# Optimization experiments

Measured on AMD Instinct MI355X. Metric: run time of the kernel, lower is better.

The kernel has to match this reference:

```python
import jax, jax.numpy as jnp
import numpy as np

ETA = 0.01   # nudging rate from __init__ default
EPS = 1e-8   # cosine-similarity epsilon


def setup_inputs() -> dict:
    key = jax.random.key(0)
    ks = jax.random.split(key, 6)
    B, F, S, E, D = 64, 512, 8192, 500000, 1024
    return {
        "heatmap_features_batch": jax.random.normal(ks[0], (B, F), dtype=jnp.float32),
        "grad_output_batch": jax.random.normal(ks[1], (B, F), dtype=jnp.float32),
        "sign_features": jax.random.normal(ks[2], (S, F), dtype=jnp.float32),
        "edge_weight": jax.random.uniform(ks[3], (E,), dtype=jnp.float32),
        "edge_disease": jax.random.randint(ks[4], (E,), 0, D, dtype=jnp.int32),
        "edge_sign": jax.random.randint(ks[5], (E,), 0, S, dtype=jnp.int32),
        "num_diseases": D,
    }


def reference(heatmap_features_batch, grad_output_batch, sign_features,
              edge_weight, edge_disease, edge_sign, num_diseases):
    # Cosine similarity between every sample's heatmap feature vector and every
    # sign node's stored feature vector, rescaled to [0, 1].
    Hn = heatmap_features_batch / (
        jnp.linalg.norm(heatmap_features_batch, axis=1, keepdims=True) + EPS)
    Sn = sign_features / (
        jnp.linalg.norm(sign_features, axis=1, keepdims=True) + EPS)
    sim = (jnp.einsum('bf,sf->bs', Hn, Sn) + 1.0) * 0.5          # [B, S]

    # Per-edge weighted similarity, gathered at each edge's sign node.
    contrib = sim[:, edge_sign] * edge_weight[None, :]           # [B, E]

    # Scatter-add edge contributions into the disease (source) index.
    agg = jax.ops.segment_sum(contrib.T, edge_disease,
                              num_segments=num_diseases)         # [D, B]

    # Per-sample gradient norm factor g^(i) = ||grad_i||_2.
    gnorm = jnp.linalg.norm(grad_output_batch, axis=1)           # [B]

    return ETA * gnorm[:, None] * agg.T                          # [B, D]
```

## Files before the change

kernel.cpp:

```cpp
#include <hip/hip_runtime.h>
#include <math.h>

#define EPS 1e-8f
#define SCB 256
#define NG  256
#define CAP 768

__global__ __launch_bounds__(256) void k_norms(
        const float* __restrict__ Sg, const float* __restrict__ Hg,
        const float* __restrict__ Gg, float* __restrict__ rinv,
        float* __restrict__ Hs, float* __restrict__ gscale,
        int* __restrict__ cursor, int Srows, int Fdim, int Bdim, int Dd) {
    int bid = blockIdx.x;
    int tid = threadIdx.x;
    int lane = tid & 63, w = tid >> 6;
    int ns4 = Srows >> 2;
    int nf4 = Fdim >> 2;

    if (bid < ns4) {
        int s = bid * 4 + w;
        const float4* p = (const float4*)(Sg + (size_t)s * Fdim);
        float4 a = p[lane], c = p[lane + 64];
        float acc = a.x * a.x + a.y * a.y + a.z * a.z + a.w * a.w
                  + c.x * c.x + c.y * c.y + c.z * c.z + c.w * c.w;
        #pragma unroll
        for (int off = 32; off; off >>= 1) acc += __shfl_xor(acc, off, 64);
        if (lane == 0) rinv[s] = 1.0f / (sqrtf(acc) + EPS);
        (void)nf4;
    } else if (bid < ns4 + (Bdim >> 2)) {
        int b = (bid - ns4) * 4 + w;
        const float4* ph = (const float4*)(Hg + (size_t)b * Fdim);
        const float4* pg = (const float4*)(Gg + (size_t)b * Fdim);
        float4 h0 = ph[lane], h1 = ph[lane + 64];
        float4 g0 = pg[lane], g1 = pg[lane + 64];
        float ah = h0.x * h0.x + h0.y * h0.y + h0.z * h0.z + h0.w * h0.w
                 + h1.x * h1.x + h1.y * h1.y + h1.z * h1.z + h1.w * h1.w;
        float ag = g0.x * g0.x + g0.y * g0.y + g0.z * g0.z + g0.w * g0.w
                 + g1.x * g1.x + g1.y * g1.y + g1.z * g1.z + g1.w * g1.w;
        #pragma unroll
        for (int off = 32; off; off >>= 1) {
            ah += __shfl_xor(ah, off, 64);
            ag += __shfl_xor(ag, off, 64);
        }
        float hn = 1.0f / (sqrtf(ah) + EPS);
        if (lane == 0) gscale[b] = 0.005f * sqrtf(ag);
        float4* dst = (float4*)(Hs + (size_t)b * Fdim);
        float4 o0, o1;
        o0.x = h0.x * hn; o0.y = h0.y * hn; o0.z = h0.z * hn; o0.w = h0.w * hn;
        o1.x = h1.x * hn; o1.y = h1.y * hn; o1.z = h1.z * hn; o1.w = h1.w * hn;
        dst[lane] = o0; dst[lane + 64] = o1;
    } else {
        for (int i = tid; i < Dd; i += 256) cursor[i] = 0;
    }
}

__global__ __launch_bounds__(256) void k_g1scat(
        const float* __restrict__ Hs, const float* __restrict__ Sg,
        const float* __restrict__ rinv, float* __restrict__ Pt,
        const int* __restrict__ ed, const int* __restrict__ es,
        const float* __restrict__ ew, int* __restrict__ cursor,
        int2* __restrict__ sorted, int Srows, int Fdim, int E, int Dd) {
    __shared__ float smem[64 * 68 + 32 * 68];
    int id = blockIdx.x;
    int tid = threadIdx.x;

    if (id < NG) {
        float (*Hl)[68] = (float(*)[68])smem;
        float (*Sl)[68] = (float(*)[68])(smem + 64 * 68);
        int lane = tid & 63, w = tid >> 6;
        int s0 = id * 32;

        float acc[8];
        #pragma unroll
        for (int i = 0; i < 8; i++) acc[i] = 0.f;

        for (int kt = 0; kt < Fdim; kt += 64) {
            #pragma unroll
            for (int i = 0; i < 4; i++) {
                int idx = tid + i * 256;
                int c = idx & 15, r = idx >> 4;
                *(float4*)&Hl[r][c * 4] =
                    *(const float4*)&Hs[(size_t)r * Fdim + kt + c * 4];
            }
            #pragma unroll
            for (int i = 0; i < 2; i++) {
                int idx = tid + i * 256;
                int c = idx & 15, r = idx >> 4;
                *(float4*)&Sl[r][c * 4] =
                    *(const float4*)&Sg[(size_t)(s0 + r) * Fdim + kt + c * 4];
            }
            __syncthreads();
            #pragma unroll
            for (int kk = 0; kk < 16; kk++) {
                float4 hv = *(float4*)&Hl[lane][kk * 4];
                #pragma unroll
                for (int si = 0; si < 8; si++) {
                    float4 sv = *(float4*)&Sl[w * 8 + si][kk * 4];
                    acc[si] += sv.x * hv.x + sv.y * hv.y
                             + sv.z * hv.z + sv.w * hv.w;
                }
            }
            __syncthreads();
        }
        #pragma unroll
        for (int si = 0; si < 8; si++) {
            int s = s0 + w * 8 + si;
            Pt[(size_t)s * 64 + lane] = acc[si] * rinv[s];
        }
    } else {
        int* cnt = (int*)smem;
        int h = id - NG;
        for (int i = tid; i < Dd; i += 256) cnt[i] = 0;
        __syncthreads();
        int chunk = (E + SCB - 1) / SCB;
        int e0 = h * chunk;
        int e1 = min(E, e0 + chunk);
        int myd[8], mys[8], myr[8];
        float myw[8];
        #pragma unroll
        for (int i = 0; i < 8; i++) {
            int e = e0 + tid + i * 256;
            myd[i] = -1;
            if (e < e1) {
                myd[i] = ed[e]; mys[i] = es[e]; myw[i] = ew[e];
                myr[i] = atomicAdd(&cnt[myd[i]], 1);
            }
        }
        __syncthreads();
        for (int d = tid; d < Dd; d += 256) {
            int c = cnt[d];
            if (c) cnt[d] = atomicAdd(&cursor[d], c);
        }
        __syncthreads();
        #pragma unroll
        for (int i = 0; i < 8; i++) {
            if (myd[i] >= 0) {
                int pos = cnt[myd[i]] + myr[i];
                sorted[(size_t)myd[i] * CAP + pos] =
                    make_int2(mys[i], __float_as_int(myw[i]));
            }
        }
    }
}

__global__ __launch_bounds__(256) void k_gather(
        const int2* __restrict__ sorted, const float* __restrict__ Pt,
        const int* __restrict__ cursor, const float* __restrict__ gscale,
        float* __restrict__ out, int Dd) {
    __shared__ float sacc[4][64];
    __shared__ float scs[4];
    int d = blockIdx.x;
    int tid = threadIdx.x;
    int lane = tid & 63, w = tid >> 6;
    int cnt = cursor[d];
    const int2* sp = sorted + (size_t)d * CAP;
    float acc = 0.f, cs = 0.f;
    #pragma unroll 8
    for (int i = w; i < cnt; i += 4) {
        int2 p = sp[i];
        float wt = __int_as_float(p.y);
        acc += wt * Pt[(size_t)p.x * 64 + lane];
        cs += wt;
    }
    sacc[w][lane] = acc;
    if (lane == 0) scs[w] = cs;
    __syncthreads();
    if (tid < 64) {
        float a = sacc[0][tid] + sacc[1][tid] + sacc[2][tid] + sacc[3][tid]
                + scs[0] + scs[1] + scs[2] + scs[3];
        out[(size_t)tid * Dd + d] = gscale[tid] * a;
    }
}

extern "C" void kernel_launch(void* const* d_in, const int* in_sizes, int n_in,
                              void* d_out, int out_size, void* d_ws, size_t ws_size,
                              hipStream_t stream) {
    const float* H  = (const float*)d_in[0];
    const float* G  = (const float*)d_in[1];
    const float* Sg = (const float*)d_in[2];
    const float* ew = (const float*)d_in[3];
    const int*   ed = (const int*)d_in[4];
    const int*   es = (const int*)d_in[5];

    const int B = 64;
    const int F = in_sizes[0] / B;
    const int S = in_sizes[2] / F;
    const int E = in_sizes[3];
    const int D = out_size / B;
    float* out = (float*)d_out;

    float* ws = (float*)d_ws;
    size_t off = 0;
    float* rinv   = ws + off; off += (size_t)S;
    float* Hs     = ws + off; off += (size_t)B * F;
    float* gscale = ws + off; off += 256;
    float* Pt     = ws + off; off += (size_t)S * B;
    int*   cursor = (int*)(ws + off); off += (size_t)D;
    int2*  sorted = (int2*)(ws + off); off += 2 * (size_t)D * CAP;

    k_norms<<<S / 4 + B / 4 + 1, 256, 0, stream>>>(Sg, H, G, rinv, Hs, gscale,
                                                   cursor, S, F, B, D);
    k_g1scat<<<NG + SCB, 256, 0, stream>>>(Hs, Sg, rinv, Pt, ed, es, ew,
                                           cursor, sorted, S, F, E, D);
    k_gather<<<D, 256, 0, stream>>>(sorted, Pt, cursor, gscale, out, D);
}
```

Before: 143.2 us.

## Use bf16 MFMA for similarity GEMM with prenormalized bf16 operands

The norms kernel now writes row-normalized sign features and heatmap features as bf16. The similarity GEMM is replaced by a matrix-core path using mfma_f32_16x16x32_bf16, with operands loaded directly from global memory instead of through an LDS-tiled FP32 FMA loop. Fewer GEMM blocks are launched, each wave computing a 16x64 tile. This removes scalar FMA work and halves operand bytes, at the cost of bf16 rounding error in the similarity values.

```diff
diff --git a/kernel.cpp b/kernel.cpp
--- a/kernel.cpp
+++ b/kernel.cpp
@@ -3,36 +3,52 @@
 
 #define EPS 1e-8f
 #define SCB 256
-#define NG  256
+#define NG1 128
 #define CAP 768
+
+typedef __attribute__((ext_vector_type(8))) __bf16 bf16x8;
+typedef __attribute__((ext_vector_type(4))) float f32x4;
+
+__device__ __forceinline__ unsigned short f2bf(float x) {
+    unsigned int u = __float_as_uint(x);
+    u += 0x7FFFu + ((u >> 16) & 1u);
+    return (unsigned short)(u >> 16);
+}
+__device__ __forceinline__ unsigned int pack2(float lo, float hi) {
+    return (unsigned int)f2bf(lo) | ((unsigned int)f2bf(hi) << 16);
+}
 
 __global__ __launch_bounds__(256) void k_norms(
         const float* __restrict__ Sg, const float* __restrict__ Hg,
-        const float* __restrict__ Gg, float* __restrict__ rinv,
-        float* __restrict__ Hs, float* __restrict__ gscale,
+        const float* __restrict__ Gg, unsigned short* __restrict__ Sgb,
+        unsigned short* __restrict__ Hsb, float* __restrict__ gscale,
         int* __restrict__ cursor, int Srows, int Fdim, int Bdim, int Dd) {
     int bid = blockIdx.x;
     int tid = threadIdx.x;
     int lane = tid & 63, w = tid >> 6;
     int ns4 = Srows >> 2;
-    int nf4 = Fdim >> 2;
 
     if (bid < ns4) {
         int s = bid * 4 + w;
         const float4* p = (const float4*)(Sg + (size_t)s * Fdim);
-        float4 a = p[lane], c = p[lane + 64];
+        float4 a = p[2 * lane], c = p[2 * lane + 1];
         float acc = a.x * a.x + a.y * a.y + a.z * a.z + a.w * a.w
                   + c.x * c.x + c.y * c.y + c.z * c.z + c.w * c.w;
         #pragma unroll
         for (int off = 32; off; off >>= 1) acc += __shfl_xor(acc, off, 64);
-        if (lane == 0) rinv[s] = 1.0f / (sqrtf(acc) + EPS);
-        (void)nf4;
+        float rv = 1.0f / (sqrtf(acc) + EPS);
+        uint4 o;
+        o.x = pack2(a.x * rv, a.y * rv);
+        o.y = pack2(a.z * rv, a.w * rv);
+        o.z = pack2(c.x * rv, c.y * rv);
+        o.w = pack2(c.z * rv, c.w * rv);
+        *(uint4*)(Sgb + (size_t)s * Fdim + lane * 8) = o;
     } else if (bid < ns4 + (Bdim >> 2)) {
         int b = (bid - ns4) * 4 + w;
         const float4* ph = (const float4*)(Hg + (size_t)b * Fdim);
         const float4* pg = (const float4*)(Gg + (size_t)b * Fdim);
-        float4 h0 = ph[lane], h1 = ph[lane + 64];
-        float4 g0 = pg[lane], g1 = pg[lane + 64];
+        float4 h0 = ph[2 * lane], h1 = ph[2 * lane + 1];
+        float4 g0 = pg[2 * lane], g1 = pg[2 * lane + 1];
         float ah = h0.x * h0.x + h0.y * h0.y + h0.z * h0.z + h0.w * h0.w
                  + h1.x * h1.x + h1.y * h1.y + h1.z * h1.z + h1.w * h1.w;
         float ag = g0.x * g0.x + g0.y * g0.y + g0.z * g0.z + g0.w * g0.w
@@ -44,72 +60,62 @@
         }
         float hn = 1.0f / (sqrtf(ah) + EPS);
         if (lane == 0) gscale[b] = 0.005f * sqrtf(ag);
-        float4* dst = (float4*)(Hs + (size_t)b * Fdim);
-        float4 o0, o1;
-        o0.x = h0.x * hn; o0.y = h0.y * hn; o0.z = h0.z * hn; o0.w = h0.w * hn;
-        o1.x = h1.x * hn; o1.y = h1.y * hn; o1.z = h1.z * hn; o1.w = h1.w * hn;
-        dst[lane] = o0; dst[lane + 64] = o1;
+        uint4 o;
+        o.x = pack2(h0.x * hn, h0.y * hn);
+        o.y = pack2(h0.z * hn, h0.w * hn);
+        o.z = pack2(h1.x * hn, h1.y * hn);
+        o.w = pack2(h1.z * hn, h1.w * hn);
+        *(uint4*)(Hsb + (size_t)b * Fdim + lane * 8) = o;
     } else {
         for (int i = tid; i < Dd; i += 256) cursor[i] = 0;
     }
 }
 
 __global__ __launch_bounds__(256) void k_g1scat(
-        const float* __restrict__ Hs, const float* __restrict__ Sg,
-        const float* __restrict__ rinv, float* __restrict__ Pt,
+        const unsigned short* __restrict__ Sgb,
+        const unsigned short* __restrict__ Hsb, float* __restrict__ Pt,
         const int* __restrict__ ed, const int* __restrict__ es,
         const float* __restrict__ ew, int* __restrict__ cursor,
         int2* __restrict__ sorted, int Srows, int Fdim, int E, int Dd) {
-    __shared__ float smem[64 * 68 + 32 * 68];
+    __shared__ int cnt[1024];
     int id = blockIdx.x;
     int tid = threadIdx.x;
 
-    if (id < NG) {
-        float (*Hl)[68] = (float(*)[68])smem;
-        float (*Sl)[68] = (float(*)[68])(smem + 64 * 68);
+    if (id < NG1) {
         int lane = tid & 63, w = tid >> 6;
-        int s0 = id * 32;
-
-        float acc[8];
-        #pragma unroll
-        for (int i = 0; i < 8; i++) acc[i] = 0.f;
-
-        for (int kt = 0; kt < Fdim; kt += 64) {
-            #pragma unroll
-            for (int i = 0; i < 4; i++) {
-                int idx = tid + i * 256;
-                int c = idx & 15, r = idx >> 4;
-                *(float4*)&Hl[r][c * 4] =
-                    *(const float4*)&Hs[(size_t)r * Fdim + kt + c * 4];
-            }
-            #pragma unroll
-            for (int i = 0; i < 2; i++) {
-                int idx = tid + i * 256;
-                int c = idx & 15, r = idx >> 4;
-                *(float4*)&Sl[r][c * 4] =
-                    *(const float4*)&Sg[(size_t)(s0 + r) * Fdim + kt + c * 4];
-            }
-            __syncthreads();
-            #pragma unroll
-            for (int kk = 0; kk < 16; kk++) {
-                float4 hv = *(float4*)&Hl[lane][kk * 4];
-                #pragma unroll
-                for (int si = 0; si < 8; si++) {
-                    float4 sv = *(float4*)&Sl[w * 8 + si][kk * 4];
-                    acc[si] += sv.x * hv.x + sv.y * hv.y
-                             + sv.z * hv.z + sv.w * hv.w;
-                }
-            }
-            __syncthreads();
-        }
-        #pragma unroll
-        for (int si = 0; si < 8; si++) {
-            int s = s0 + w * 8 + si;
-            Pt[(size_t)s * 64 + lane] = acc[si] * rinv[s];
+        int r16 = lane & 15, q = lane >> 4;
+        int s0 = (id * 4 + w) * 16;
+        const bf16x8* Ap = (const bf16x8*)(Sgb + (size_t)(s0 + r16) * Fdim) + q;
+        const bf16x8* Bp = (const bf16x8*)(Hsb + (size_t)r16 * Fdim) + q;
+
+        f32x4 acc0 = {0.f, 0.f, 0.f, 0.f};
+        f32x4 acc1 = {0.f, 0.f, 0.f, 0.f};
+        f32x4 acc2 = {0.f, 0.f, 0.f, 0.f};
+        f32x4 acc3 = {0.f, 0.f, 0.f, 0.f};
+
+        #pragma unroll 4
+        for (int kt = 0; kt < 16; kt++) {
+            bf16x8 a  = Ap[kt * 4];
+            bf16x8 b0 = Bp[kt * 4];
+            bf16x8 b1 = Bp[kt * 4 + 16 * 64];
+            bf16x8 b2 = Bp[kt * 4 + 32 * 64];
+            bf16x8 b3 = Bp[kt * 4 + 48 * 64];
+            acc0 = __builtin_amdgcn_mfma_f32_16x16x32_bf16(a, b0, acc0, 0, 0, 0);
+            acc1 = __builtin_amdgcn_mfma_f32_16x16x32_bf16(a, b1, acc1, 0, 0, 0);
+            acc2 = __builtin_amdgcn_mfma_f32_16x16x32_bf16(a, b2, acc2, 0, 0, 0);
+            acc3 = __builtin_amdgcn_mfma_f32_16x16x32_bf16(a, b3, acc3, 0, 0, 0);
+        }
+        #pragma unroll
+        for (int r = 0; r < 4; r++) {
+            int s = s0 + q * 4 + r;
+            float* row = Pt + (size_t)s * 64 + r16;
+            row[0]  = acc0[r];
+            row[16] = acc1[r];
+            row[32] = acc2[r];
+            row[48] = acc3[r];
         }
     } else {
-        int* cnt = (int*)smem;
-        int h = id - NG;
+        int h = id - NG1;
         for (int i = tid; i < Dd; i += 256) cnt[i] = 0;
         __syncthreads();
         int chunk = (E + SCB - 1) / SCB;
@@ -191,16 +197,16 @@
 
     float* ws = (float*)d_ws;
     size_t off = 0;
-    float* rinv   = ws + off; off += (size_t)S;
-    float* Hs     = ws + off; off += (size_t)B * F;
+    unsigned short* Sgb = (unsigned short*)(ws + off); off += (size_t)S * F / 2;
+    unsigned short* Hsb = (unsigned short*)(ws + off); off += (size_t)B * F / 2;
     float* gscale = ws + off; off += 256;
     float* Pt     = ws + off; off += (size_t)S * B;
     int*   cursor = (int*)(ws + off); off += (size_t)D;
     int2*  sorted = (int2*)(ws + off); off += 2 * (size_t)D * CAP;
 
-    k_norms<<<S / 4 + B / 4 + 1, 256, 0, stream>>>(Sg, H, G, rinv, Hs, gscale,
+    k_norms<<<S / 4 + B / 4 + 1, 256, 0, stream>>>(Sg, H, G, Sgb, Hsb, gscale,
                                                    cursor, S, F, B, D);
-    k_g1scat<<<NG + SCB, 256, 0, stream>>>(Hs, Sg, rinv, Pt, ed, es, ew,
-                                           cursor, sorted, S, F, E, D);
+    k_g1scat<<<NG1 + SCB, 256, 0, stream>>>(Sgb, Hsb, Pt, ed, es, ew,
+                                            cursor, sorted, S, F, E, D);
     k_gather<<<D, 256, 0, stream>>>(sorted, Pt, cursor, gscale, out, D);
 }
```

Result: faster. 118.2 us, median of 2 (-17.4%).
